# Kernel optimization log

Measured on AMD Instinct MI355X. Metric: run time of the kernel, lower is better.

## Reference

```python
import jax, jax.numpy as jnp
import numpy as np

TEMPERATURE = 0.5
N, D = 8192, 512
NUM_CLASSES = 1000


def setup_inputs() -> dict:
    key = jax.random.key(0)
    k0, k1, k2 = jax.random.split(key, 3)
    out0 = jax.random.normal(k0, (N, D), dtype=jnp.float32)
    out1 = jax.random.normal(k1, (N, D), dtype=jnp.float32)
    labels = jax.random.randint(k2, (N,), 0, NUM_CLASSES, dtype=jnp.int64)
    return {"out0": out0, "out1": out1, "labels": labels}


def _l2_normalize(x, eps=1e-12):
    # matches torch F.normalize(dim=1): x / max(||x||, eps)
    norm = jnp.sqrt(jnp.sum(x * x, axis=1, keepdims=True))
    return x / jnp.maximum(norm, eps)


def reference(out0, out1, labels):
    out0 = _l2_normalize(out0)
    out1 = _l2_normalize(out1)
    logits = jnp.matmul(out0, out1.T) / TEMPERATURE          # [N, N]
    logits_exp = jnp.exp(logits)                             # [N, N]
    positive_mask = (labels[:, None] == labels[None, :])     # [N, N] bool
    pos_sum = jnp.sum(jnp.where(positive_mask, logits_exp, 0.0), axis=1)  # [N]
    all_sum = jnp.sum(logits_exp, axis=1)                    # [N]
    loss = -jnp.mean(jnp.log(pos_sum / all_sum))
    return loss
```

## Files before the change

### kernel.cpp

```cpp
#include <hip/hip_runtime.h>

using f32x4  = __attribute__((ext_vector_type(4))) float;
using f32x16 = __attribute__((ext_vector_type(16))) float;
using i32x8  = __attribute__((ext_vector_type(8))) int;

constexpr int   N = 8192;
constexpr int   D = 512;
constexpr float SCALE_FOLD = 1.6986436f;
constexpr int   CGROUPS = 64;

static __device__ __forceinline__ void gld16(const unsigned char* g, unsigned char* l) {
  __builtin_amdgcn_global_load_lds(
      (const __attribute__((address_space(1))) void*)g,
      (__attribute__((address_space(3))) void*)l, 16, 0, 0);
}

__global__ __launch_bounds__(256) void normalize_kernel(
    const float* __restrict__ in0, const float* __restrict__ in1,
    unsigned char* __restrict__ n0, unsigned char* __restrict__ n1) {
  int gw   = (blockIdx.x * 256 + threadIdx.x) >> 6;
  int lane = threadIdx.x & 63;
  int row  = (gw < N) ? gw : gw - N;
  const float* src = (gw < N) ? in0 + (size_t)row * D : in1 + (size_t)row * D;
  unsigned char* dstrow = (gw < N) ? n0 + (size_t)row * D : n1 + (size_t)row * D;

  const float4* s4 = reinterpret_cast<const float4*>(src) + (size_t)lane * 2;
  float4 v0 = s4[0], v1 = s4[1];
  float ss = v0.x*v0.x + v0.y*v0.y + v0.z*v0.z + v0.w*v0.w
           + v1.x*v1.x + v1.y*v1.y + v1.z*v1.z + v1.w*v1.w;
#pragma unroll
  for (int m = 1; m <= 32; m <<= 1) ss += __shfl_xor(ss, m);
  float s = SCALE_FOLD / fmaxf(sqrtf(ss), 1e-12f);

  int w0 = 0, w1 = 0;
  w0 = __builtin_amdgcn_cvt_pk_fp8_f32(v0.x * s, v0.y * s, w0, false);
  w0 = __builtin_amdgcn_cvt_pk_fp8_f32(v0.z * s, v0.w * s, w0, true);
  w1 = __builtin_amdgcn_cvt_pk_fp8_f32(v1.x * s, v1.y * s, w1, false);
  w1 = __builtin_amdgcn_cvt_pk_fp8_f32(v1.z * s, v1.w * s, w1, true);
  int2 o; o.x = w0; o.y = w1;

  const int c  = (row >> 1) & 3;
  const int k8 = lane & 7;
  const int g  = k8 >> 1, h = k8 & 1;
  const int off = (lane >> 3) * 64 + ((g ^ c) * 16) + h * 8;
  *reinterpret_cast<int2*>(dstrow + off) = o;
}

__global__ __launch_bounds__(256, 4) void ntxent_main(
    const unsigned char* __restrict__ n0, const unsigned char* __restrict__ n1,
    const int* __restrict__ labels,
    float* __restrict__ part_pos, float* __restrict__ part_all) {
  __shared__ unsigned char As[2][128 * 64];
  __shared__ unsigned char Bs[2][128 * 64];
  __shared__ float redS[256];
  __shared__ int   labC[128];

  const int t    = threadIdx.x;
  const int lane = t & 63;
  const int wid  = t >> 6;
  const int l31  = lane & 31;
  const int hi   = lane >> 5;
  const int wr   = wid >> 1;
  const int wc   = wid & 1;

  const int swz = (blockIdx.x & 7) * 512 + (blockIdx.x >> 3);
  const int rowtile = swz >> 6;
  const int colgrp  = swz & 63;
  const int rowbase = rowtile * 128;
  const int colb    = colgrp * 128;

  if (t < 128) labC[t] = labels[colb + t];

  const unsigned char* gA = n0 + (size_t)(rowbase + (t >> 2)) * D + (t & 3) * 16;
  const unsigned char* gB = n1 + (size_t)(colb    + (t >> 2)) * D + (t & 3) * 16;
  unsigned char* const lA = &As[0][0] + (t >> 2) * 64 + (t & 3) * 16;
  unsigned char* const lB = &Bs[0][0] + (t >> 2) * 64 + (t & 3) * 16;

#define STAGE(st, sb) do { \
    const unsigned char* _ga = gA + (st) * 64; \
    const unsigned char* _gb = gB + (st) * 64; \
    unsigned char* _la = lA + (sb) * 8192; \
    unsigned char* _lb = lB + (sb) * 8192; \
    gld16(_ga, _la); gld16(_ga + (size_t)64 * D, _la + 4096); \
    gld16(_gb, _lb); gld16(_gb + (size_t)64 * D, _lb + 4096); \
  } while (0)

  int aoff[2], boff[2];
#pragma unroll
  for (int mi = 0; mi < 2; ++mi) {
    int tr = wr * 64 + mi * 32 + l31;
    aoff[mi] = tr * 64 + (((hi << 1) ^ ((tr >> 1) & 3)) << 4);
  }
#pragma unroll
  for (int ji = 0; ji < 2; ++ji) {
    int tc = wc * 64 + ji * 32 + l31;
    boff[ji] = tc * 64 + (((hi << 1) ^ ((tc >> 1) & 3)) << 4);
  }

#define GATE4 asm volatile("s_waitcnt vmcnt(4)\n\ts_barrier" ::: "memory")
#define GATE0 asm volatile("s_waitcnt vmcnt(0)\n\ts_barrier" ::: "memory")
#define BARP  asm volatile("s_barrier" ::: "memory")
#define EBAR  asm volatile("s_waitcnt lgkmcnt(0)\n\ts_barrier" ::: "memory")

  const int sc1 = 0x7f7f7f7f;

  f32x16 acc[2][2];
#pragma unroll
  for (int ji = 0; ji < 2; ++ji)
#pragma unroll
    for (int mi = 0; mi < 2; ++mi) acc[ji][mi] = 0.f;

  STAGE(0, 0);
  STAGE(1, 1);

#pragma unroll
  for (int kk = 0; kk < 8; ++kk) {
    if (kk < 7) { GATE4; } else { GATE0; }

    const unsigned char* bufA = &As[kk & 1][0];
    const unsigned char* bufB = &Bs[kk & 1][0];
    i32x8 a[2], b[2];
#pragma unroll
    for (int mi = 0; mi < 2; ++mi) {
      int4 lo = *(const int4*)&bufA[aoff[mi]];
      int4 hh = *(const int4*)&bufA[aoff[mi] ^ 16];
      a[mi] = (i32x8){lo.x, lo.y, lo.z, lo.w, hh.x, hh.y, hh.z, hh.w};
    }
#pragma unroll
    for (int ji = 0; ji < 2; ++ji) {
      int4 lo = *(const int4*)&bufB[boff[ji]];
      int4 hh = *(const int4*)&bufB[boff[ji] ^ 16];
      b[ji] = (i32x8){lo.x, lo.y, lo.z, lo.w, hh.x, hh.y, hh.z, hh.w};
    }

    __builtin_amdgcn_s_setprio(1);
#pragma unroll
    for (int ji = 0; ji < 2; ++ji)
#pragma unroll
      for (int mi = 0; mi < 2; ++mi)
        acc[ji][mi] = __builtin_amdgcn_mfma_scale_f32_32x32x64_f8f6f4(
            b[ji], a[mi], acc[ji][mi], 0, 0, 0, sc1, 0, sc1);
    __builtin_amdgcn_s_setprio(0);

    if (kk < 6) { BARP; STAGE(kk + 2, kk & 1); }
  }

  int labi[2];
#pragma unroll
  for (int mi = 0; mi < 2; ++mi)
    labi[mi] = labels[rowbase + wr * 64 + mi * 32 + l31];

  float asum[2] = {0.f, 0.f};
  float psum[2] = {0.f, 0.f};
#pragma unroll
  for (int ji = 0; ji < 2; ++ji)
#pragma unroll
    for (int rq = 0; rq < 4; ++rq) {
      const int4 labj = *(const int4*)&labC[wc * 64 + ji * 32 + rq * 8 + 4 * hi];
#pragma unroll
      for (int mi = 0; mi < 2; ++mi)
#pragma unroll
        for (int rr = 0; rr < 4; ++rr) {
          float e = exp2f(acc[ji][mi][rq * 4 + rr]);
          asum[mi] += e;
          int lb = (rr == 0) ? labj.x : (rr == 1) ? labj.y : (rr == 2) ? labj.z : labj.w;
          if (lb == labi[mi]) psum[mi] += e;
        }
    }

#pragma unroll
  for (int mi = 0; mi < 2; ++mi) {
    asum[mi] += __shfl_xor(asum[mi], 32);
    psum[mi] += __shfl_xor(psum[mi], 32);
  }

  float* redSa = redS;
  float* redSp = redS + 128;
  if (wc == 1 && hi == 0) {
#pragma unroll
    for (int mi = 0; mi < 2; ++mi) {
      redSa[wr * 64 + mi * 32 + l31] = asum[mi];
      redSp[wr * 64 + mi * 32 + l31] = psum[mi];
    }
  }
  EBAR;
  if (wc == 0 && hi == 0) {
#pragma unroll
    for (int mi = 0; mi < 2; ++mi) {
      const int idx = wr * 64 + mi * 32 + l31;
      const int row = rowbase + idx;
      part_all[(size_t)colgrp * N + row] = asum[mi] + redSa[idx];
      part_pos[(size_t)colgrp * N + row] = psum[mi] + redSp[idx];
    }
  }
}

__global__ __launch_bounds__(256) void row_reduce(
    const float* __restrict__ part_pos, const float* __restrict__ part_all,
    float* __restrict__ blocksum) {
  const int i = blockIdx.x * 256 + threadIdx.x;
  float a = 0.f, p = 0.f;
#pragma unroll 4
  for (int cs = 0; cs < CGROUPS; ++cs) {
    a += part_all[(size_t)cs * N + i];
    p += part_pos[(size_t)cs * N + i];
  }
  float s = logf(a) - logf(p);
  __shared__ float red[256];
  red[threadIdx.x] = s;
  __syncthreads();
  for (int off = 128; off > 0; off >>= 1) {
    if (threadIdx.x < off) red[threadIdx.x] += red[threadIdx.x + off];
    __syncthreads();
  }
  if (threadIdx.x == 0) blocksum[blockIdx.x] = red[0];
}

__global__ __launch_bounds__(64) void final_sum(
    const float* __restrict__ blocksum, float* __restrict__ out) {
  float s = (threadIdx.x < N / 256) ? blocksum[threadIdx.x] : 0.f;
#pragma unroll
  for (int m = 1; m <= 32; m <<= 1) s += __shfl_xor(s, m);
  if (threadIdx.x == 0) out[0] = s / (float)N;
}

extern "C" void kernel_launch(void* const* d_in, const int* in_sizes, int n_in,
                              void* d_out, int out_size, void* d_ws, size_t ws_size,
                              hipStream_t stream) {
  const float* out0   = (const float*)d_in[0];
  const float* out1   = (const float*)d_in[1];
  const int*   labels = (const int*)d_in[2];
  float*       out    = (float*)d_out;

  char* ws = (char*)d_ws;
  unsigned char* n0 = (unsigned char*)ws;
  unsigned char* n1 = (unsigned char*)(ws + (size_t)N * D);
  float* part_pos = (float*)(ws + (size_t)2 * N * D);
  float* part_all = part_pos + (size_t)CGROUPS * N;
  float* blocksum = part_all + (size_t)CGROUPS * N;

  hipLaunchKernelGGL(normalize_kernel, dim3(2 * N / 4), dim3(256), 0, stream,
                     out0, out1, n0, n1);
  hipLaunchKernelGGL(ntxent_main, dim3(4096), dim3(256), 0, stream,
                     n0, n1, labels, part_pos, part_all);
  hipLaunchKernelGGL(row_reduce, dim3(N / 256), dim3(256), 0, stream,
                     part_pos, part_all, blocksum);
  hipLaunchKernelGGL(final_sum, dim3(1), dim3(64), 0, stream,
                     blocksum, out);
}
```

Before: 66.75 us.

## Process two column tiles per block, prefetching the second tile during the first epilogue

```diff
diff --git a/kernel.cpp b/kernel.cpp
--- a/kernel.cpp
+++ b/kernel.cpp
@@ -1,6 +1,5 @@
 #include <hip/hip_runtime.h>
 
-using f32x4  = __attribute__((ext_vector_type(4))) float;
 using f32x16 = __attribute__((ext_vector_type(16))) float;
 using i32x8  = __attribute__((ext_vector_type(8))) int;
 
@@ -8,6 +7,12 @@
 constexpr int   D = 512;
 constexpr float SCALE_FOLD = 1.6986436f;
 constexpr int   CGROUPS = 64;
+
+#if __has_builtin(__builtin_amdgcn_exp2f)
+#define EXP2(x) __builtin_amdgcn_exp2f(x)
+#else
+#define EXP2(x) exp2f(x)
+#endif
 
 static __device__ __forceinline__ void gld16(const unsigned char* g, unsigned char* l) {
   __builtin_amdgcn_global_load_lds(
@@ -53,7 +58,7 @@
   __shared__ unsigned char As[2][128 * 64];
   __shared__ unsigned char Bs[2][128 * 64];
   __shared__ float redS[256];
-  __shared__ int   labC[128];
+  __shared__ int   labC[256];
 
   const int t    = threadIdx.x;
   const int lane = t & 63;
@@ -63,24 +68,25 @@
   const int wr   = wid >> 1;
   const int wc   = wid & 1;
 
-  const int swz = (blockIdx.x & 7) * 512 + (blockIdx.x >> 3);
-  const int rowtile = swz >> 6;
-  const int colgrp  = swz & 63;
+  const int swz = (blockIdx.x & 7) * 256 + (blockIdx.x >> 3);
+  const int rowtile = swz >> 5;
+  const int colpair = swz & 31;
   const int rowbase = rowtile * 128;
-  const int colb    = colgrp * 128;
-
-  if (t < 128) labC[t] = labels[colb + t];
+  const int colb    = colpair * 256;
+
+  labC[t] = labels[colb + t];
 
   const unsigned char* gA = n0 + (size_t)(rowbase + (t >> 2)) * D + (t & 3) * 16;
   const unsigned char* gB = n1 + (size_t)(colb    + (t >> 2)) * D + (t & 3) * 16;
   unsigned char* const lA = &As[0][0] + (t >> 2) * 64 + (t & 3) * 16;
   unsigned char* const lB = &Bs[0][0] + (t >> 2) * 64 + (t & 3) * 16;
 
-#define STAGE(st, sb) do { \
-    const unsigned char* _ga = gA + (st) * 64; \
-    const unsigned char* _gb = gB + (st) * 64; \
-    unsigned char* _la = lA + (sb) * 8192; \
-    unsigned char* _lb = lB + (sb) * 8192; \
+#define STAGE(st) do { \
+    const int _sb = (st) & 1; \
+    const unsigned char* _ga = gA + ((st) & 7) * 64; \
+    const unsigned char* _gb = gB + (size_t)(((st) >> 3) * 128) * D + ((st) & 7) * 64; \
+    unsigned char* _la = lA + _sb * 8192; \
+    unsigned char* _lb = lB + _sb * 8192; \
     gld16(_ga, _la); gld16(_ga + (size_t)64 * D, _la + 4096); \
     gld16(_gb, _lb); gld16(_gb + (size_t)64 * D, _lb + 4096); \
   } while (0)
@@ -110,27 +116,80 @@
 #pragma unroll
     for (int mi = 0; mi < 2; ++mi) acc[ji][mi] = 0.f;
 
-  STAGE(0, 0);
-  STAGE(1, 1);
-
-#pragma unroll
-  for (int kk = 0; kk < 8; ++kk) {
-    if (kk < 7) { GATE4; } else { GATE0; }
+  auto epilogue = [&](int tt) {
+    int labi[2];
+#pragma unroll
+    for (int mi = 0; mi < 2; ++mi)
+      labi[mi] = labels[rowbase + wr * 64 + mi * 32 + l31];
+    float asum[2] = {0.f, 0.f};
+    float psum[2] = {0.f, 0.f};
+#pragma unroll
+    for (int ji = 0; ji < 2; ++ji)
+#pragma unroll
+      for (int rq = 0; rq < 4; ++rq) {
+        const int4 labj = *(const int4*)&labC[tt * 128 + wc * 64 + ji * 32 + rq * 8 + 4 * hi];
+#pragma unroll
+        for (int mi = 0; mi < 2; ++mi)
+#pragma unroll
+          for (int rr = 0; rr < 4; ++rr) {
+            float e = EXP2(acc[ji][mi][rq * 4 + rr]);
+            asum[mi] += e;
+            int lb = (rr == 0) ? labj.x : (rr == 1) ? labj.y : (rr == 2) ? labj.z : labj.w;
+            if (lb == labi[mi]) psum[mi] += e;
+          }
+      }
+#pragma unroll
+    for (int mi = 0; mi < 2; ++mi) {
+      asum[mi] += __shfl_xor(asum[mi], 32);
+      psum[mi] += __shfl_xor(psum[mi], 32);
+    }
+    float* redSa = redS;
+    float* redSp = redS + 128;
+    if (wc == 1 && hi == 0) {
+#pragma unroll
+      for (int mi = 0; mi < 2; ++mi) {
+        redSa[wr * 64 + mi * 32 + l31] = asum[mi];
+        redSp[wr * 64 + mi * 32 + l31] = psum[mi];
+      }
+    }
+    EBAR;
+    const int cg = colpair * 2 + tt;
+    if (wc == 0 && hi == 0) {
+#pragma unroll
+      for (int mi = 0; mi < 2; ++mi) {
+        const int idx = wr * 64 + mi * 32 + l31;
+        const int row = rowbase + idx;
+        part_all[(size_t)cg * N + row] = asum[mi] + redSa[idx];
+        part_pos[(size_t)cg * N + row] = psum[mi] + redSp[idx];
+      }
+    }
+#pragma unroll
+    for (int ji = 0; ji < 2; ++ji)
+#pragma unroll
+      for (int mi = 0; mi < 2; ++mi) acc[ji][mi] = 0.f;
+  };
+
+  STAGE(0);
+  STAGE(1);
+
+#pragma unroll
+  for (int kk = 0; kk < 16; ++kk) {
+    if (kk < 15) { GATE4; } else { GATE0; }
 
     const unsigned char* bufA = &As[kk & 1][0];
     const unsigned char* bufB = &Bs[kk & 1][0];
     i32x8 a[2], b[2];
 #pragma unroll
     for (int mi = 0; mi < 2; ++mi) {
-      int4 lo = *(const int4*)&bufA[aoff[mi]];
-      int4 hh = *(const int4*)&bufA[aoff[mi] ^ 16];
-      a[mi] = (i32x8){lo.x, lo.y, lo.z, lo.w, hh.x, hh.y, hh.z, hh.w};
+      int4* pa = (int4*)&a[mi];
+      pa[0] = *(const int4*)&bufA[aoff[mi]];
+      pa[1] = *(const int4*)&bufA[aoff[mi] ^ 16];
     }
 #pragma unroll
     for (int ji = 0; ji < 2; ++ji) {
-      int4 lo = *(const int4*)&bufB[boff[ji]];
-      int4 hh = *(const int4*)&bufB[boff[ji] ^ 16];
-      b[ji] = (i32x8){lo.x, lo.y, lo.z, lo.w, hh.x, hh.y, hh.z, hh.w};
+      int4* pb = (int4*)&b[ji];
+      pb[0] = *(const int4*)&bufB[boff[ji]];
+      pb[1] = *(const int4*)&bufB[boff[ji] ^ 16];
     }
 
     __builtin_amdgcn_s_setprio(1);
@@ -142,57 +201,10 @@
             b[ji], a[mi], acc[ji][mi], 0, 0, 0, sc1, 0, sc1);
     __builtin_amdgcn_s_setprio(0);
 
-    if (kk < 6) { BARP; STAGE(kk + 2, kk & 1); }
-  }
-
-  int labi[2];
-#pragma unroll
-  for (int mi = 0; mi < 2; ++mi)
-    labi[mi] = labels[rowbase + wr * 64 + mi * 32 + l31];
-
-  float asum[2] = {0.f, 0.f};
-  float psum[2] = {0.f, 0.f};
-#pragma unroll
-  for (int ji = 0; ji < 2; ++ji)
-#pragma unroll
-    for (int rq = 0; rq < 4; ++rq) {
-      const int4 labj = *(const int4*)&labC[wc * 64 + ji * 32 + rq * 8 + 4 * hi];
-#pragma unroll
-      for (int mi = 0; mi < 2; ++mi)
-#pragma unroll
-        for (int rr = 0; rr < 4; ++rr) {
-          float e = exp2f(acc[ji][mi][rq * 4 + rr]);
-          asum[mi] += e;
-          int lb = (rr == 0) ? labj.x : (rr == 1) ? labj.y : (rr == 2) ? labj.z : labj.w;
-          if (lb == labi[mi]) psum[mi] += e;
-        }
-    }
-
-#pragma unroll
-  for (int mi = 0; mi < 2; ++mi) {
-    asum[mi] += __shfl_xor(asum[mi], 32);
-    psum[mi] += __shfl_xor(psum[mi], 32);
-  }
-
-  float* redSa = redS;
-  float* redSp = redS + 128;
-  if (wc == 1 && hi == 0) {
-#pragma unroll
-    for (int mi = 0; mi < 2; ++mi) {
-      redSa[wr * 64 + mi * 32 + l31] = asum[mi];
-      redSp[wr * 64 + mi * 32 + l31] = psum[mi];
-    }
-  }
-  EBAR;
-  if (wc == 0 && hi == 0) {
-#pragma unroll
-    for (int mi = 0; mi < 2; ++mi) {
-      const int idx = wr * 64 + mi * 32 + l31;
-      const int row = rowbase + idx;
-      part_all[(size_t)colgrp * N + row] = asum[mi] + redSa[idx];
-      part_pos[(size_t)colgrp * N + row] = psum[mi] + redSp[idx];
-    }
-  }
+    if (kk < 14) { BARP; STAGE(kk + 2); }
+    if (kk == 7) epilogue(0);
+  }
+  epilogue(1);
 }
 
 __global__ __launch_bounds__(256) void row_reduce(
@@ -241,7 +253,7 @@
 
   hipLaunchKernelGGL(normalize_kernel, dim3(2 * N / 4), dim3(256), 0, stream,
                      out0, out1, n0, n1);
-  hipLaunchKernelGGL(ntxent_main, dim3(4096), dim3(256), 0, stream,
+  hipLaunchKernelGGL(ntxent_main, dim3(2048), dim3(256), 0, stream,
                      n0, n1, labels, part_pos, part_all);
   hipLaunchKernelGGL(row_reduce, dim3(N / 256), dim3(256), 0, stream,
                      part_pos, part_all, blocksum);
```

After: 72.62 us. +8.8%, slower.
